# Optimization experiments

Measured on AMD Instinct MI355X. Metric: run time of the kernel, lower is better.

The kernel has to match this reference:

```python
import jax, jax.numpy as jnp
import numpy as np

EMBED = 768; HEADS = 12; DH = 64; DEPTH = 6; MLP = 3072
PATCH = (4, 16, 16)
N_PATCH = 2048          # (32/4)*(256/16)*(256/16)
N_REAL = N_PATCH + 1    # + cls token
S_PAD = 4096            # padded to multiple of max segment length
SEGS = [128, 256, 512, 1024, 2048]
RATIOS = [1, 2, 4, 8, 16]
NEG = -1e9


def _ln(x, w, b, eps=1e-5):
    m = jnp.mean(x, -1, keepdims=True)
    v = jnp.mean((x - m) ** 2, -1, keepdims=True)
    return (x - m) / jnp.sqrt(v + eps) * w + b


def dilated_attn(x, wq, bq, wk, bk, wv, bv, wo, bo):
    """LongNet dilated attention: per (segment w, ratio r) branch, split the
    sequence into segments of length w, keep every r-th token with a per-head
    offset (h % r), run dense attention inside the sparse segment, then combine
    branches per position/head with softmax-denominator (lse) weights."""
    B, S, E = x.shape
    q = (x @ wq + bq).reshape(B, S, HEADS, DH)
    k = (x @ wk + bk).reshape(B, S, HEADS, DH)
    v = (x @ wv + bv).reshape(B, S, HEADS, DH)
    scale = 1.0 / np.sqrt(DH).astype(np.float32)
    harr = jnp.arange(HEADS)[:, None]
    outs, lses = [], []
    for w, r in zip(SEGS, RATIOS):
        ns, m = S // w, w // r
        idx = (jnp.arange(HEADS)[:, None] % r) + r * jnp.arange(m)[None, :]  # [H, m]

        def seg(t):
            t = t.reshape(B, ns, w, HEADS, DH).transpose(0, 1, 3, 2, 4)  # B,ns,H,w,D
            return jnp.take_along_axis(t, idx[None, None, :, :, None], axis=3)

        qs, ks, vs = seg(q), seg(k), seg(v)  # [B, ns, H, m, D]
        pos = (jnp.arange(ns) * w)[:, None, None] + idx[None]  # [ns, H, m]
        kmask = jnp.where(pos < N_REAL, 0.0, NEG)  # mask padded keys
        sc = jnp.einsum('bnhqd,bnhkd->bnhqk', qs, ks) * scale + kmask[None, :, :, None, :]
        lse = jax.nn.logsumexp(sc, axis=-1)  # [B, ns, H, m]
        o = jnp.einsum('bnhqk,bnhkd->bnhqd', jax.nn.softmax(sc, axis=-1), vs)
        of = jnp.zeros((B, ns, HEADS, w, DH), x.dtype).at[:, :, harr, idx, :].set(o)
        lf = jnp.full((B, ns, HEADS, w), NEG, x.dtype).at[:, :, harr, idx].set(lse)
        outs.append(of.transpose(0, 1, 3, 2, 4).reshape(B, S, HEADS, DH))
        lses.append(lf.transpose(0, 1, 3, 2).reshape(B, S, HEADS))
    O = jnp.stack(outs)   # [Br, B, S, H, D]
    L = jnp.stack(lses)   # [Br, B, S, H]
    wts = jnp.exp(L - jnp.max(L, 0))
    wts = wts / jnp.sum(wts, 0)
    out = jnp.sum(O * wts[..., None], 0).reshape(B, S, E)
    return out @ wo + bo


def setup_inputs() -> dict:
    key = jax.random.key(0)
    ks = jax.random.split(key, 16)
    f = lambda k, shape: (0.02 * jax.random.normal(k, shape)).astype(jnp.float32)
    z = lambda *s: jnp.zeros(s, jnp.float32)
    o = lambda *s: jnp.ones(s, jnp.float32)
    return {
        'x': jax.random.normal(ks[0], (1, 1, 32, 256, 256), dtype=jnp.float32),
        'conv_w': f(ks[1], (EMBED, 1) + PATCH),
        'conv_b': z(EMBED),
        'cls_token': f(ks[2], (1, 1, EMBED)),
        'pos_embed': f(ks[3], (1, N_REAL, EMBED)),
        'ln1_w': o(DEPTH, EMBED), 'ln1_b': z(DEPTH, EMBED),
        'wq': f(ks[4], (DEPTH, EMBED, EMBED)), 'bq': z(DEPTH, EMBED),
        'wk': f(ks[5], (DEPTH, EMBED, EMBED)), 'bk': z(DEPTH, EMBED),
        'wv': f(ks[6], (DEPTH, EMBED, EMBED)), 'bv': z(DEPTH, EMBED),
        'wo': f(ks[7], (DEPTH, EMBED, EMBED)), 'bo': z(DEPTH, EMBED),
        'ln2_w': o(DEPTH, EMBED), 'ln2_b': z(DEPTH, EMBED),
        'w1': f(ks[8], (DEPTH, EMBED, MLP)), 'b1': z(DEPTH, MLP),
        'w2': f(ks[9], (DEPTH, MLP, EMBED)), 'b2': z(DEPTH, EMBED),
        'lnf_w': o(EMBED), 'lnf_b': z(EMBED),
    }


def reference(x, conv_w, conv_b, cls_token, pos_embed, ln1_w, ln1_b,
              wq, bq, wk, bk, wv, bv, wo, bo, ln2_w, ln2_b,
              w1, b1, w2, b2, lnf_w, lnf_b):
    # 3D patch embed: Conv3d stride=kernel=patch, then flatten spatial -> tokens
    p = jax.lax.conv_general_dilated(
        x, conv_w, window_strides=PATCH, padding='VALID',
        dimension_numbers=('NCDHW', 'OIDHW', 'NCDHW'))
    p = p + conv_b[None, :, None, None, None]
    B = p.shape[0]
    tok = p.reshape(B, EMBED, -1).transpose(0, 2, 1)  # [B, N_PATCH, E]
    tok = tok + pos_embed[:, 1:, :]
    cls = cls_token + pos_embed[:, :1, :]
    h = jnp.concatenate([jnp.broadcast_to(cls, (B, 1, EMBED)), tok], axis=1)
    h = jnp.pad(h, ((0, 0), (0, S_PAD - N_REAL), (0, 0)))  # pad to segment multiple

    params = {'ln1_w': ln1_w, 'ln1_b': ln1_b, 'wq': wq, 'bq': bq, 'wk': wk,
              'bk': bk, 'wv': wv, 'bv': bv, 'wo': wo, 'bo': bo,
              'ln2_w': ln2_w, 'ln2_b': ln2_b, 'w1': w1, 'b1': b1,
              'w2': w2, 'b2': b2}

    def layer(h, pr):
        a = dilated_attn(_ln(h, pr['ln1_w'], pr['ln1_b']),
                         pr['wq'], pr['bq'], pr['wk'], pr['bk'],
                         pr['wv'], pr['bv'], pr['wo'], pr['bo'])
        h = h + a
        f = _ln(h, pr['ln2_w'], pr['ln2_b'])
        f = jax.nn.gelu(f @ pr['w1'] + pr['b1'], approximate=False) @ pr['w2'] + pr['b2']
        return h + f, None

    h, _ = jax.lax.scan(layer, h, params)
    return _ln(h[:, 0], lnf_w, lnf_b)  # [B, EMBED]
```

## Files before the change

### kernel.cpp

```cpp
#include <hip/hip_runtime.h>
#include <math.h>

#define EMBED 768
#define HEADS 12
#define DH 64
#define DEPTH 6
#define MLP_DIM 3072
#define N_REAL 2049
#define SP 2112
#define SPAD 2176
#define NEGV (-1e9f)

typedef __attribute__((ext_vector_type(8))) short short8;
typedef __attribute__((ext_vector_type(4))) float f32x4;

__device__ __forceinline__ unsigned short f2bf(float f) {
    union { float f; unsigned u; } x; x.f = f;
    unsigned r = x.u + 0x7FFF + ((x.u >> 16) & 1);
    return (unsigned short)(r >> 16);
}
__device__ __forceinline__ float bf2f(unsigned short s) {
    union { unsigned u; float f; } x; x.u = (unsigned)s << 16;
    return x.f;
}

__device__ __forceinline__ size_t pidx(int mj, int k, int nkt) {
    return (((size_t)(mj >> 4) * nkt + (k >> 5)) << 9) + (size_t)((((k >> 3) & 3) * 16 + (mj & 15)) * 8 + (k & 7));
}

__global__ void im2col_kernel(const float* __restrict__ x, unsigned short* __restrict__ p) {
    const int pi = blockIdx.x;
    const int d = pi >> 8, rr = (pi >> 4) & 15, cc = pi & 15;
    const int t = threadIdx.x;
    #pragma unroll
    for (int u = 0; u < 4; ++u) {
        int i = u * 256 + t;
        int kd = i >> 8, kr = (i >> 4) & 15, kc = i & 15;
        float v = x[(size_t)(d * 4 + kd) * 65536 + (rr * 16 + kr) * 256 + (cc * 16 + kc)];
        p[pidx(pi, i, 32)] = f2bf(v);
    }
}

__global__ void pack_KN_kernel(const float* __restrict__ src, unsigned short* __restrict__ dst,
                               int N, int K) {
    __shared__ float lf[128][33];
    const int bn = blockIdx.x, bk = blockIdx.y;
    const int t = threadIdx.x;
    {
        const int kk = t >> 3, ch = t & 7;
        const float4* s = (const float4*)(src + (size_t)(bk * 32 + kk) * N + bn * 128 + ch * 16);
        float4 v0 = s[0], v1 = s[1], v2 = s[2], v3 = s[3];
        float tmp[16];
        ((float4*)tmp)[0] = v0; ((float4*)tmp)[1] = v1; ((float4*)tmp)[2] = v2; ((float4*)tmp)[3] = v3;
        #pragma unroll
        for (int u = 0; u < 16; ++u) lf[ch * 16 + u][kk] = tmp[u];
    }
    __syncthreads();
    const int nkt = K >> 5;
    const int cg = t >> 5;
    const int l0 = (t & 31) * 2;
    unsigned short* o = dst + (((size_t)(bn * 8 + cg) * nkt + bk) << 9);
    #pragma unroll
    for (int q = 0; q < 2; ++q) {
        const int l = l0 + q;
        const int col = cg * 16 + (l & 15), kb = (l >> 4) * 8;
        unsigned short ov[8];
        #pragma unroll
        for (int e = 0; e < 8; ++e) ov[e] = f2bf(lf[col][kb + e]);
        *(short8*)(o + l * 8) = *(short8*)ov;
    }
}

__global__ void pack_NK_kernel(const float* __restrict__ src, unsigned short* __restrict__ dst,
                               int N, int K) {
    __shared__ float lf[128][33];
    const int bn = blockIdx.x, bk = blockIdx.y;
    const int t = threadIdx.x;
    {
        const int row = t >> 1, hf = t & 1;
        const float4* s = (const float4*)(src + (size_t)(bn * 128 + row) * K + bk * 32 + hf * 16);
        float4 v0 = s[0], v1 = s[1], v2 = s[2], v3 = s[3];
        float tmp[16];
        ((float4*)tmp)[0] = v0; ((float4*)tmp)[1] = v1; ((float4*)tmp)[2] = v2; ((float4*)tmp)[3] = v3;
        #pragma unroll
        for (int u = 0; u < 16; ++u) lf[row][hf * 16 + u] = tmp[u];
    }
    __syncthreads();
    const int nkt = K >> 5;
    const int cg = t >> 5;
    const int l0 = (t & 31) * 2;
    unsigned short* o = dst + (((size_t)(bn * 8 + cg) * nkt + bk) << 9);
    #pragma unroll
    for (int q = 0; q < 2; ++q) {
        const int l = l0 + q;
        const int col = cg * 16 + (l & 15), kb = (l >> 4) * 8;
        unsigned short ov[8];
        #pragma unroll
        for (int e = 0; e < 8; ++e) ov[e] = f2bf(lf[col][kb + e]);
        *(short8*)(o + l * 8) = *(short8*)ov;
    }
}

__global__ void concat_bias_kernel(const float* __restrict__ bq, const float* __restrict__ bk,
                                   const float* __restrict__ bv, float* __restrict__ bqkv) {
    int i = blockIdx.x * 256 + threadIdx.x;
    if (i >= DEPTH * 2304) return;
    int L = i / 2304, j = i - L * 2304;
    float v = (j < 768) ? bq[L * 768 + j] : (j < 1536) ? bk[L * 768 + j - 768] : bv[L * 768 + j - 1536];
    bqkv[i] = v;
}

__global__ void cls_init_kernel(const float* __restrict__ cls,
                                const float* __restrict__ pos,
                                float* __restrict__ h) {
    int e = blockIdx.x * 256 + threadIdx.x;
    if (e < EMBED) h[e] = cls[e] + pos[e];
}

template<bool PACKED>
__global__ void ln_kernel(const float* __restrict__ in, void* __restrict__ outv,
                          const float* __restrict__ w, const float* __restrict__ b,
                          int M) {
    int row = blockIdx.x;
    if (row >= M) return;
    const float* xr = in + (size_t)row * EMBED;
    int tid = threadIdx.x;
    float v0 = xr[tid], v1 = xr[tid + 256], v2 = xr[tid + 512];
    __shared__ float red[4];
    float s = v0 + v1 + v2;
    #pragma unroll
    for (int o = 32; o > 0; o >>= 1) s += __shfl_down(s, o);
    if ((tid & 63) == 0) red[tid >> 6] = s;
    __syncthreads();
    float mean = (red[0] + red[1] + red[2] + red[3]) * (1.0f / 768.0f);
    __syncthreads();
    float d0 = v0 - mean, d1 = v1 - mean, d2 = v2 - mean;
    float q2 = d0 * d0 + d1 * d1 + d2 * d2;
    #pragma unroll
    for (int o = 32; o > 0; o >>= 1) q2 += __shfl_down(q2, o);
    if ((tid & 63) == 0) red[tid >> 6] = q2;
    __syncthreads();
    float var = (red[0] + red[1] + red[2] + red[3]) * (1.0f / 768.0f);
    float rstd = 1.0f / sqrtf(var + 1e-5f);
    float o0 = d0 * rstd * w[tid]       + b[tid];
    float o1 = d1 * rstd * w[tid + 256] + b[tid + 256];
    float o2 = d2 * rstd * w[tid + 512] + b[tid + 512];
    if (PACKED) {
        unsigned short* o = (unsigned short*)outv;
        o[pidx(row, tid,       24)] = f2bf(o0);
        o[pidx(row, tid + 256, 24)] = f2bf(o1);
        o[pidx(row, tid + 512, 24)] = f2bf(o2);
    } else {
        float* orow = (float*)outv + (size_t)row * EMBED;
        orow[tid] = o0; orow[tid + 256] = o1; orow[tid + 512] = o2;
    }
}

template<int ACT, int MODE>
__global__ __launch_bounds__(64)
void gemm_bf16(const unsigned short* __restrict__ Apk, const unsigned short* __restrict__ Bpk,
               const float* __restrict__ bias, void* __restrict__ Cv,
               int M, int N, int K) {
    const int lane = threadIdx.x;
    const int row0 = blockIdx.y * 64, col0 = blockIdx.x * 64;
    const int nkt = K >> 5;

    f32x4 acc[4][4];
    #pragma unroll
    for (int mi = 0; mi < 4; ++mi)
        #pragma unroll
        for (int ni = 0; ni < 4; ++ni)
            #pragma unroll
            for (int j = 0; j < 4; ++j) acc[mi][ni][j] = 0.0f;

    const unsigned short* Ab[4];
    const unsigned short* Bb[4];
    #pragma unroll
    for (int i = 0; i < 4; ++i) {
        Ab[i] = Apk + (((size_t)(blockIdx.y * 4 + i) * nkt) << 9) + lane * 8;
        Bb[i] = Bpk + (((size_t)(blockIdx.x * 4 + i) * nkt) << 9) + lane * 8;
    }

    short8 a0[4], b0[4], a1[4], b1[4];
    auto LOADT = [&](int t, short8* aa, short8* bb) {
        #pragma unroll
        for (int i = 0; i < 4; ++i) {
            aa[i] = *(const short8*)(Ab[i] + (size_t)t * 512);
            bb[i] = *(const short8*)(Bb[i] + (size_t)t * 512);
        }
    };
    auto MF = [&](short8* aa, short8* bb) {
        #pragma unroll
        for (int mi = 0; mi < 4; ++mi)
            #pragma unroll
            for (int ni = 0; ni < 4; ++ni)
                acc[mi][ni] = __builtin_amdgcn_mfma_f32_16x16x32_bf16(aa[mi], bb[ni], acc[mi][ni], 0, 0, 0);
    };

    LOADT(0, a0, b0);
    for (int t = 0; t < nkt; t += 2) {
        LOADT(t + 1, a1, b1);
        MF(a0, b0);
        if (t + 2 < nkt) LOADT(t + 2, a0, b0);
        MF(a1, b1);
    }

    float* Cf = (float*)Cv;
    unsigned short* Cb = (unsigned short*)Cv;
    const int ln15 = lane & 15, kq = lane >> 4;
    const int nktN = N >> 5;
    #pragma unroll
    for (int mi = 0; mi < 4; ++mi) {
        #pragma unroll
        for (int ni = 0; ni < 4; ++ni) {
            const int col = col0 + ni * 16 + ln15;
            const float bb = bias[col];
            #pragma unroll
            for (int j = 0; j < 4; ++j) {
                const int row = row0 + mi * 16 + kq * 4 + j;
                if (row < M) {
                    float v = acc[mi][ni][j] + bb;
                    if (ACT == 1) v = 0.5f * v * (1.0f + erff(v * 0.70710678118654752f));
                    if (MODE == 1)      Cf[(size_t)row * N + col] += v;
                    else if (MODE == 2) Cb[(size_t)row * N + col] = f2bf(v);
                    else                Cb[pidx(row, col, nktN)] = f2bf(v);
                }
            }
        }
    }
}

__global__ __launch_bounds__(256, 1)
void attn_kernel(const unsigned short* __restrict__ qkv,
                 unsigned short* __restrict__ Obr, float* __restrict__ Lbr) {
    const int bx = blockIdx.x, hh = blockIdx.y;
    int b, n;
    if      (bx < 17) { b = 0; n = bx; }
    else if (bx < 26) { b = 1; n = bx - 17; }
    else if (bx < 31) { b = 2; n = bx - 26; }
    else if (bx < 34) { b = 3; n = bx - 31; }
    else              { b = 4; n = bx - 34; }
    const int r = 1 << b;
    const int segw = 128 << b;
    const int base = n * segw + (hh & (r - 1));

    __shared__ __attribute__((aligned(16))) unsigned short VT[64 * 128];
    __shared__ __attribute__((aligned(16))) unsigned short Pl[128 * 128];

    const int tid = threadIdx.x;

    {
        const int key = tid >> 1, dh2 = (tid & 1) * 32;
        const int pos = base + r * key;
        const bool val = pos < N_REAL;
        const unsigned short* vsrc = qkv + (size_t)(val ? pos : 0) * 2304 + 1536 + hh * 64 + dh2;
        #pragma unroll
        for (int u = 0; u < 4; ++u) {
            short8 vv = ((const short8*)vsrc)[u];
            #pragma unroll
            for (int e = 0; e < 8; ++e) {
                const int d = dh2 + u * 8 + e;
                VT[(d * 256 + ((key * 2) ^ ((d & 7) << 4))) >> 1] =
                    val ? (unsigned short)vv[e] : (unsigned short)0;
            }
        }
    }
    __syncthreads();

    const int lane = tid & 63, wv = tid >> 6;
    const int ln15 = lane & 15, kq = lane >> 4;

    f32x4 sc[2][8];
    #pragma unroll
    for (int mi = 0; mi < 2; ++mi)
        #pragma unroll
        for (int ni = 0; ni < 8; ++ni)
            #pragma unroll
            for (int j = 0; j < 4; ++j) sc[mi][ni][j] = 0.0f;

    #pragma unroll
    for (int kt = 0; kt < 2; ++kt) {
        short8 qfr[2], kfr[8];
        #pragma unroll
        for (int mi = 0; mi < 2; ++mi) {
            const int pos = base + r * (wv * 32 + mi * 16 + ln15);
            qfr[mi] = *(const short8*)(qkv + (size_t)(pos < N_REAL ? pos : 0) * 2304
                                       + hh * 64 + kt * 32 + kq * 8);
        }
        #pragma unroll
        for (int ni = 0; ni < 8; ++ni) {
            const int pos = base + r * (ni * 16 + ln15);
            kfr[ni] = *(const short8*)(qkv + (size_t)(pos < N_REAL ? pos : 0) * 2304
                                       + 768 + hh * 64 + kt * 32 + kq * 8);
        }
        #pragma unroll
        for (int mi = 0; mi < 2; ++mi)
            #pragma unroll
            for (int ni = 0; ni < 8; ++ni)
                sc[mi][ni] = __builtin_amdgcn_mfma_f32_16x16x32_bf16(qfr[mi], kfr[ni], sc[mi][ni], 0, 0, 0);
    }

    #pragma unroll
    for (int ni = 0; ni < 8; ++ni) {
        const bool kval = (base + r * (ni * 16 + ln15)) < N_REAL;
        #pragma unroll
        for (int mi = 0; mi < 2; ++mi)
            #pragma unroll
            for (int j = 0; j < 4; ++j)
                sc[mi][ni][j] = kval ? sc[mi][ni][j] * 0.125f : NEGV;
    }

    float rsum[2][4];
    #pragma unroll
    for (int mi = 0; mi < 2; ++mi) {
        #pragma unroll
        for (int j = 0; j < 4; ++j) {
            float mx = sc[mi][0][j];
            #pragma unroll
            for (int ni = 1; ni < 8; ++ni) mx = fmaxf(mx, sc[mi][ni][j]);
            mx = fmaxf(mx, __shfl_xor(mx, 1));
            mx = fmaxf(mx, __shfl_xor(mx, 2));
            mx = fmaxf(mx, __shfl_xor(mx, 4));
            mx = fmaxf(mx, __shfl_xor(mx, 8));
            float sm = 0.f;
            #pragma unroll
            for (int ni = 0; ni < 8; ++ni) {
                float e = __expf(sc[mi][ni][j] - mx);
                sc[mi][ni][j] = e;
                sm += e;
            }
            sm += __shfl_xor(sm, 1);
            sm += __shfl_xor(sm, 2);
            sm += __shfl_xor(sm, 4);
            sm += __shfl_xor(sm, 8);
            rsum[mi][j] = sm;
            const int prow = wv * 32 + mi * 16 + kq * 4 + j;
            const int qpos = base + r * prow;
            if (ln15 == 0 && qpos < N_REAL)
                Lbr[((size_t)b * SP + qpos) * HEADS + hh] = mx + logf(sm);
        }
    }

    #pragma unroll
    for (int mi = 0; mi < 2; ++mi)
        #pragma unroll
        for (int j = 0; j < 4; ++j) {
            const int prow = wv * 32 + mi * 16 + kq * 4 + j;
            #pragma unroll
            for (int ni = 0; ni < 8; ++ni) {
                const int col = ni * 16 + ln15;
                Pl[(prow * 256 + ((col * 2) ^ ((prow & 7) << 4))) >> 1] = f2bf(sc[mi][ni][j]);
            }
        }
    __syncthreads();

    f32x4 ov[2][4];
    #pragma unroll
    for (int mi = 0; mi < 2; ++mi)
        #pragma unroll
        for (int ni = 0; ni < 4; ++ni)
            #pragma unroll
            for (int j = 0; j < 4; ++j) ov[mi][ni][j] = 0.0f;

    #pragma unroll
    for (int kt = 0; kt < 4; ++kt) {
        short8 pa[2], vb[4];
        #pragma unroll
        for (int mi = 0; mi < 2; ++mi) {
            const int row = wv * 32 + mi * 16 + ln15;
            pa[mi] = *(const short8*)((const char*)Pl + row * 256
                                      + ((kt * 64 + kq * 16) ^ ((row & 7) << 4)));
        }
        #pragma unroll
        for (int ni = 0; ni < 4; ++ni) {
            const int d = ni * 16 + ln15;
            vb[ni] = *(const short8*)((const char*)VT + d * 256
                                      + ((kt * 64 + kq * 16) ^ ((d & 7) << 4)));
        }
        #pragma unroll
        for (int mi = 0; mi < 2; ++mi)
            #pragma unroll
            for (int ni = 0; ni < 4; ++ni)
                ov[mi][ni] = __builtin_amdgcn_mfma_f32_16x16x32_bf16(pa[mi], vb[ni], ov[mi][ni], 0, 0, 0);
    }

    #pragma unroll
    for (int mi = 0; mi < 2; ++mi)
        #pragma unroll
        for (int j = 0; j < 4; ++j) {
            const int prow = wv * 32 + mi * 16 + kq * 4 + j;
            const int qpos = base + r * prow;
            if (qpos < N_REAL) {
                const float inv = 1.0f / rsum[mi][j];
                #pragma unroll
                for (int ni = 0; ni < 4; ++ni)
                    Obr[((size_t)b * N_REAL + qpos) * EMBED + hh * 64 + ni * 16 + ln15] =
                        f2bf(ov[mi][ni][j] * inv);
            }
        }
}

__global__ void combine_kernel(const unsigned short* __restrict__ Obr, const float* __restrict__ Lbr,
                               unsigned short* __restrict__ out) {
    int gid = blockIdx.x * 256 + threadIdx.x;
    if (gid >= N_REAL * EMBED) return;
    int p = gid / EMBED, e = gid - p * EMBED;
    int h = e >> 6;
    float l[5];
    float mx = NEGV;
    #pragma unroll
    for (int b = 0; b < 5; ++b) {
        const int rm = (1 << b) - 1;
        l[b] = ((p & rm) == (h & rm)) ? Lbr[((size_t)b * SP + p) * HEADS + h] : NEGV;
        mx = fmaxf(mx, l[b]);
    }
    float wsum = 0.f, acc = 0.f;
    #pragma unroll
    for (int b = 0; b < 5; ++b) {
        if (l[b] > NEGV * 0.5f) {
            float wt = expf(l[b] - mx);
            wsum += wt;
            acc += wt * bf2f(Obr[((size_t)b * N_REAL + p) * EMBED + e]);
        }
    }
    out[pidx(p, e, 24)] = f2bf(acc / wsum);
}

extern "C" void kernel_launch(void* const* d_in, const int* in_sizes, int n_in,
                              void* d_out, int out_size, void* d_ws, size_t ws_size,
                              hipStream_t stream) {
    const float* x      = (const float*)d_in[0];
    const float* conv_w = (const float*)d_in[1];
    const float* conv_b = (const float*)d_in[2];
    const float* cls    = (const float*)d_in[3];
    const float* pos    = (const float*)d_in[4];
    const float* ln1w   = (const float*)d_in[5];
    const float* ln1b   = (const float*)d_in[6];
    const float* wq     = (const float*)d_in[7];
    const float* bq     = (const float*)d_in[8];
    const float* wk     = (const float*)d_in[9];
    const float* bk     = (const float*)d_in[10];
    const float* wv     = (const float*)d_in[11];
    const float* bv     = (const float*)d_in[12];
    const float* wo     = (const float*)d_in[13];
    const float* bo     = (const float*)d_in[14];
    const float* ln2w   = (const float*)d_in[15];
    const float* ln2b   = (const float*)d_in[16];
    const float* w1     = (const float*)d_in[17];
    const float* b1     = (const float*)d_in[18];
    const float* w2     = (const float*)d_in[19];
    const float* b2     = (const float*)d_in[20];
    const float* lnfw   = (const float*)d_in[21];
    const float* lnfb   = (const float*)d_in[22];

    float* ws = (float*)d_ws;
    float* h     = ws;  ws += (size_t)SP * EMBED;
    float* Lbr   = ws;  ws += (size_t)5 * SP * HEADS;
    float* bqkv  = ws;  ws += (size_t)DEPTH * 2304;
    unsigned short* qkv_bf   = (unsigned short*)ws;  ws += (size_t)SPAD * 2304 / 2;
    unsigned short* xln_pk   = (unsigned short*)ws;  ws += (size_t)SPAD * EMBED / 2;
    unsigned short* attn_pk  = (unsigned short*)ws;  ws += (size_t)SPAD * EMBED / 2;
    unsigned short* mid_pk   = (unsigned short*)ws;  ws += (size_t)SPAD * MLP_DIM / 2;
    unsigned short* patch_pk = (unsigned short*)ws;  ws += (size_t)2048 * 1024 / 2;
    unsigned short* convw_pk = (unsigned short*)ws;  ws += (size_t)EMBED * 1024 / 2;
    unsigned short* Obr      = (unsigned short*)ws;  ws += (size_t)5 * N_REAL * EMBED / 2 + 64;
    unsigned short* wqkv_pk  = (unsigned short*)ws;  ws += (size_t)2304 * EMBED / 2;
    unsigned short* wo_pk    = (unsigned short*)ws;  ws += (size_t)EMBED * EMBED / 2;
    unsigned short* w1_pk    = (unsigned short*)ws;  ws += (size_t)MLP_DIM * EMBED / 2;
    unsigned short* w2_pk    = (unsigned short*)ws;  ws += (size_t)EMBED * MLP_DIM / 2;

    im2col_kernel<<<2048, 256, 0, stream>>>(x, patch_pk);
    pack_NK_kernel<<<dim3(6, 32), 256, 0, stream>>>(conv_w, convw_pk, EMBED, 1024);
    concat_bias_kernel<<<(DEPTH * 2304 + 255) / 256, 256, 0, stream>>>(bq, bk, bv, bqkv);
    cls_init_kernel<<<3, 256, 0, stream>>>(cls, pos, h);
    hipMemcpyAsync(h + EMBED, pos + EMBED, (size_t)2048 * EMBED * sizeof(float),
                   hipMemcpyDeviceToDevice, stream);
    gemm_bf16<0, 1><<<dim3(12, 32), 64, 0, stream>>>(patch_pk, convw_pk, conv_b,
                                                     h + EMBED, 2048, EMBED, 1024);

    const size_t EEpk = (size_t)EMBED * EMBED;

    for (int L = 0; L < DEPTH; ++L) {
        const size_t EE = (size_t)EMBED * EMBED;
        const size_t EM = (size_t)EMBED * MLP_DIM;
        pack_KN_kernel<<<dim3(6, 24),  256, 0, stream>>>(wq + L * EE, wqkv_pk,            EMBED, EMBED);
        pack_KN_kernel<<<dim3(6, 24),  256, 0, stream>>>(wk + L * EE, wqkv_pk + EEpk,     EMBED, EMBED);
        pack_KN_kernel<<<dim3(6, 24),  256, 0, stream>>>(wv + L * EE, wqkv_pk + 2 * EEpk, EMBED, EMBED);
        pack_KN_kernel<<<dim3(6, 24),  256, 0, stream>>>(wo + L * EE, wo_pk,              EMBED, EMBED);
        pack_KN_kernel<<<dim3(24, 24), 256, 0, stream>>>(w1 + L * EM, w1_pk,              MLP_DIM, EMBED);
        pack_KN_kernel<<<dim3(6, 96),  256, 0, stream>>>(w2 + L * EM, w2_pk,              EMBED, MLP_DIM);

        ln_kernel<true><<<N_REAL, 256, 0, stream>>>(h, xln_pk, ln1w + (size_t)L * EMBED,
                                                    ln1b + (size_t)L * EMBED, N_REAL);
        gemm_bf16<0, 2><<<dim3(36, 33), 64, 0, stream>>>(xln_pk, wqkv_pk, bqkv + (size_t)L * 2304,
                                                         qkv_bf, N_REAL, 2304, EMBED);
        attn_kernel<<<dim3(36, 12), 256, 0, stream>>>(qkv_bf, Obr, Lbr);
        combine_kernel<<<((N_REAL * EMBED) + 255) / 256, 256, 0, stream>>>(Obr, Lbr, attn_pk);
        gemm_bf16<0, 1><<<dim3(12, 33), 64, 0, stream>>>(attn_pk, wo_pk, bo + (size_t)L * EMBED,
                                                         h, N_REAL, EMBED, EMBED);
        ln_kernel<true><<<N_REAL, 256, 0, stream>>>(h, xln_pk, ln2w + (size_t)L * EMBED,
                                                    ln2b + (size_t)L * EMBED, N_REAL);
        gemm_bf16<1, 3><<<dim3(48, 33), 64, 0, stream>>>(xln_pk, w1_pk, b1 + (size_t)L * MLP_DIM,
                                                         mid_pk, N_REAL, MLP_DIM, EMBED);
        gemm_bf16<0, 1><<<dim3(12, 33), 64, 0, stream>>>(mid_pk, w2_pk, b2 + (size_t)L * EMBED,
                                                         h, N_REAL, EMBED, MLP_DIM);
    }

    ln_kernel<false><<<1, 256, 0, stream>>>(h, (float*)d_out, lnfw, lnfb, 1);
}
```

Baseline: 1.129 ms.

## Split-K residual GEMMs with atomic accumulation, deeper prefetch, fused weight packing

The residual-add GEMMs (patch embed, output projection, MLP down-projection) now split the K dimension across gridDim.z slices and accumulate into the fp32 residual with atomicAdd, adding bias only in slice 0. This raises the block count for the narrow N=768 GEMMs, which otherwise launch few 64-thread blocks on a large GPU. The GEMM main loop now prefetches with four register buffers instead of two, and the four per-layer attention weight pack kernels are merged into one launch. The costs are atomic traffic, a summation order that can vary between runs, and higher register pressure from the deeper buffering.

```diff
diff --git a/kernel.cpp b/kernel.cpp
--- a/kernel.cpp
+++ b/kernel.cpp
@@ -41,10 +41,10 @@
     }
 }
 
-__global__ void pack_KN_kernel(const float* __restrict__ src, unsigned short* __restrict__ dst,
-                               int N, int K) {
+__device__ __forceinline__ void pack_KN_body(const float* __restrict__ src,
+                                             unsigned short* __restrict__ dst,
+                                             int N, int K, int bn, int bk) {
     __shared__ float lf[128][33];
-    const int bn = blockIdx.x, bk = blockIdx.y;
     const int t = threadIdx.x;
     {
         const int kk = t >> 3, ch = t & 7;
@@ -69,6 +69,20 @@
         for (int e = 0; e < 8; ++e) ov[e] = f2bf(lf[col][kb + e]);
         *(short8*)(o + l * 8) = *(short8*)ov;
     }
+}
+
+__global__ void pack_KN_kernel(const float* __restrict__ src, unsigned short* __restrict__ dst,
+                               int N, int K) {
+    pack_KN_body(src, dst, N, K, blockIdx.x, blockIdx.y);
+}
+
+__global__ void pack_KN4_kernel(const float* __restrict__ wq, const float* __restrict__ wk,
+                                const float* __restrict__ wv, const float* __restrict__ wo,
+                                unsigned short* __restrict__ qkv_pk, unsigned short* __restrict__ o_pk) {
+    const int z = blockIdx.z;
+    const float* src = (z == 0) ? wq : (z == 1) ? wk : (z == 2) ? wv : wo;
+    unsigned short* dst = (z < 3) ? qkv_pk + (size_t)z * EMBED * EMBED : o_pk;
+    pack_KN_body(src, dst, EMBED, EMBED, blockIdx.x, blockIdx.y);
 }
 
 __global__ void pack_NK_kernel(const float* __restrict__ src, unsigned short* __restrict__ dst,
@@ -163,7 +177,9 @@
                int M, int N, int K) {
     const int lane = threadIdx.x;
     const int row0 = blockIdx.y * 64, col0 = blockIdx.x * 64;
-    const int nkt = K >> 5;
+    const int nktT = K >> 5;
+    const int nk = nktT / gridDim.z;
+    const int t0 = blockIdx.z * nk;
 
     f32x4 acc[4][4];
     #pragma unroll
@@ -177,11 +193,10 @@
     const unsigned short* Bb[4];
     #pragma unroll
     for (int i = 0; i < 4; ++i) {
-        Ab[i] = Apk + (((size_t)(blockIdx.y * 4 + i) * nkt) << 9) + lane * 8;
-        Bb[i] = Bpk + (((size_t)(blockIdx.x * 4 + i) * nkt) << 9) + lane * 8;
-    }
-
-    short8 a0[4], b0[4], a1[4], b1[4];
+        Ab[i] = Apk + (((size_t)(blockIdx.y * 4 + i) * nktT + t0) << 9) + lane * 8;
+        Bb[i] = Bpk + (((size_t)(blockIdx.x * 4 + i) * nktT + t0) << 9) + lane * 8;
+    }
+
     auto LOADT = [&](int t, short8* aa, short8* bb) {
         #pragma unroll
         for (int i = 0; i < 4; ++i) {
@@ -197,31 +212,39 @@
                 acc[mi][ni] = __builtin_amdgcn_mfma_f32_16x16x32_bf16(aa[mi], bb[ni], acc[mi][ni], 0, 0, 0);
     };
 
-    LOADT(0, a0, b0);
-    for (int t = 0; t < nkt; t += 2) {
-        LOADT(t + 1, a1, b1);
-        MF(a0, b0);
-        if (t + 2 < nkt) LOADT(t + 2, a0, b0);
-        MF(a1, b1);
+    short8 A0[4], B0[4], A1[4], B1[4], A2[4], B2[4], A3[4], B3[4];
+    LOADT(0, A0, B0);
+    LOADT(1, A1, B1);
+    LOADT(2, A2, B2);
+    for (int t = 0; t < nk; t += 4) {
+        LOADT(t + 3, A3, B3);
+        MF(A0, B0);
+        if (t + 4 < nk) LOADT(t + 4, A0, B0);
+        MF(A1, B1);
+        if (t + 5 < nk) LOADT(t + 5, A1, B1);
+        MF(A2, B2);
+        if (t + 6 < nk) LOADT(t + 6, A2, B2);
+        MF(A3, B3);
     }
 
     float* Cf = (float*)Cv;
     unsigned short* Cb = (unsigned short*)Cv;
     const int ln15 = lane & 15, kq = lane >> 4;
     const int nktN = N >> 5;
+    const bool addb = (blockIdx.z == 0);
     #pragma unroll
     for (int mi = 0; mi < 4; ++mi) {
         #pragma unroll
         for (int ni = 0; ni < 4; ++ni) {
             const int col = col0 + ni * 16 + ln15;
-            const float bb = bias[col];
+            const float bb = addb ? bias[col] : 0.0f;
             #pragma unroll
             for (int j = 0; j < 4; ++j) {
                 const int row = row0 + mi * 16 + kq * 4 + j;
                 if (row < M) {
                     float v = acc[mi][ni][j] + bb;
                     if (ACT == 1) v = 0.5f * v * (1.0f + erff(v * 0.70710678118654752f));
-                    if (MODE == 1)      Cf[(size_t)row * N + col] += v;
+                    if (MODE == 1)      atomicAdd(&Cf[(size_t)row * N + col], v);
                     else if (MODE == 2) Cb[(size_t)row * N + col] = f2bf(v);
                     else                Cb[pidx(row, col, nktN)] = f2bf(v);
                 }
@@ -475,20 +498,17 @@
     cls_init_kernel<<<3, 256, 0, stream>>>(cls, pos, h);
     hipMemcpyAsync(h + EMBED, pos + EMBED, (size_t)2048 * EMBED * sizeof(float),
                    hipMemcpyDeviceToDevice, stream);
-    gemm_bf16<0, 1><<<dim3(12, 32), 64, 0, stream>>>(patch_pk, convw_pk, conv_b,
-                                                     h + EMBED, 2048, EMBED, 1024);
-
-    const size_t EEpk = (size_t)EMBED * EMBED;
+    gemm_bf16<0, 1><<<dim3(12, 32, 4), 64, 0, stream>>>(patch_pk, convw_pk, conv_b,
+                                                        h + EMBED, 2048, EMBED, 1024);
 
     for (int L = 0; L < DEPTH; ++L) {
         const size_t EE = (size_t)EMBED * EMBED;
         const size_t EM = (size_t)EMBED * MLP_DIM;
-        pack_KN_kernel<<<dim3(6, 24),  256, 0, stream>>>(wq + L * EE, wqkv_pk,            EMBED, EMBED);
-        pack_KN_kernel<<<dim3(6, 24),  256, 0, stream>>>(wk + L * EE, wqkv_pk + EEpk,     EMBED, EMBED);
-        pack_KN_kernel<<<dim3(6, 24),  256, 0, stream>>>(wv + L * EE, wqkv_pk + 2 * EEpk, EMBED, EMBED);
-        pack_KN_kernel<<<dim3(6, 24),  256, 0, stream>>>(wo + L * EE, wo_pk,              EMBED, EMBED);
-        pack_KN_kernel<<<dim3(24, 24), 256, 0, stream>>>(w1 + L * EM, w1_pk,              MLP_DIM, EMBED);
-        pack_KN_kernel<<<dim3(6, 96),  256, 0, stream>>>(w2 + L * EM, w2_pk,              EMBED, MLP_DIM);
+        pack_KN4_kernel<<<dim3(6, 24, 4), 256, 0, stream>>>(wq + L * EE, wk + L * EE,
+                                                            wv + L * EE, wo + L * EE,
+                                                            wqkv_pk, wo_pk);
+        pack_KN_kernel<<<dim3(24, 24), 256, 0, stream>>>(w1 + L * EM, w1_pk, MLP_DIM, EMBED);
+        pack_KN_kernel<<<dim3(6, 96),  256, 0, stream>>>(w2 + L * EM, w2_pk, EMBED, MLP_DIM);
 
         ln_kernel<true><<<N_REAL, 256, 0, stream>>>(h, xln_pk, ln1w + (size_t)L * EMBED,
                                                     ln1b + (size_t)L * EMBED, N_REAL);
@@ -496,14 +516,14 @@
                                                          qkv_bf, N_REAL, 2304, EMBED);
         attn_kernel<<<dim3(36, 12), 256, 0, stream>>>(qkv_bf, Obr, Lbr);
         combine_kernel<<<((N_REAL * EMBED) + 255) / 256, 256, 0, stream>>>(Obr, Lbr, attn_pk);
-        gemm_bf16<0, 1><<<dim3(12, 33), 64, 0, stream>>>(attn_pk, wo_pk, bo + (size_t)L * EMBED,
-                                                         h, N_REAL, EMBED, EMBED);
+        gemm_bf16<0, 1><<<dim3(12, 33, 2), 64, 0, stream>>>(attn_pk, wo_pk, bo + (size_t)L * EMBED,
+                                                            h, N_REAL, EMBED, EMBED);
         ln_kernel<true><<<N_REAL, 256, 0, stream>>>(h, xln_pk, ln2w + (size_t)L * EMBED,
                                                     ln2b + (size_t)L * EMBED, N_REAL);
         gemm_bf16<1, 3><<<dim3(48, 33), 64, 0, stream>>>(xln_pk, w1_pk, b1 + (size_t)L * MLP_DIM,
                                                          mid_pk, N_REAL, MLP_DIM, EMBED);
-        gemm_bf16<0, 1><<<dim3(12, 33), 64, 0, stream>>>(mid_pk, w2_pk, b2 + (size_t)L * EMBED,
-                                                         h, N_REAL, EMBED, MLP_DIM);
+        gemm_bf16<0, 1><<<dim3(12, 33, 4), 64, 0, stream>>>(mid_pk, w2_pk, b2 + (size_t)L * EMBED,
+                                                            h, N_REAL, EMBED, MLP_DIM);
     }
 
     ln_kernel<false><<<1, 256, 0, stream>>>(h, (float*)d_out, lnfw, lnfb, 1);
```

Result: slower. 1.408 ms (+24.7%).
